# Kernel optimization log

Hardware: AMD Instinct MI355X
Metric: run time of the kernel (lower is better)

## Reference

```python
import jax, jax.numpy as jnp
import numpy as np

# Module hyperparameters (from init_kwargs / config defaults)
LOCAL_WINDOW = 128
GLOBAL_BUDGET = 64
ATT_BUDGET = 0.05
RANDOM_BUDGET = 0.1

B, S, D = 4, 4096, 1024


def setup_inputs() -> dict:
    key = jax.random.key(0)
    k1, k2 = jax.random.split(key)
    return {
        "hidden_states": jax.random.normal(k1, (B, S, D), dtype=jnp.float32),
        "attention_mask": jnp.ones((B, S), dtype=jnp.int32),
        "W_imp": jax.random.normal(k2, (1, D), dtype=jnp.float32) * 0.02,
    }


def _build_sparse_mask(hidden_states, attention_mask, W_imp):
    b, s, d = hidden_states.shape
    valid = attention_mask.astype(bool)                       # [b, s]
    # base mask: valid x valid, with causal constraint (is_decoder=True)
    i = jnp.arange(s)[:, None]
    j = jnp.arange(s)[None, :]
    causal = j <= i                                            # [s, s]
    base = (valid[:, None, :] & valid[:, :, None]) & causal[None]

    # 1) local causal sliding window: query i attends keys in [i-W+1, i]
    diff = i - j
    local = (diff >= 0) & (diff < LOCAL_WINDOW)                # [s, s]
    sparse = jnp.broadcast_to(local[None], (b, s, s))
    selected = jnp.broadcast_to(local.any(axis=0)[None], (b, s))

    # 2) global tokens via importance projection + top-k
    base_budget = min(GLOBAL_BUDGET, max(1, int(s * ATT_BUDGET)))
    scores = jnp.einsum('bsd,d->bs', hidden_states, W_imp[0])  # [b, s]
    scores = jnp.where(valid, scores, -jnp.inf)
    _, top_idx = jax.lax.top_k(scores, base_budget)            # [b, k]
    global_tokens = jnp.zeros((b, s), bool).at[
        jnp.arange(b)[:, None], top_idx].set(True)             # [b, s]
    # globals attend to everything and are attended by everything
    sparse = sparse | global_tokens[:, None, :] | global_tokens[:, :, None]
    selected = selected | global_tokens

    # 3) structured random tokens: deterministic strided selection
    r_budget = min(s, max(1, int(s * RANDOM_BUDGET)))
    stride = max(1, s // r_budget)
    rand_idx = (jnp.arange(r_budget) * stride) % s
    random_1d = jnp.zeros((s,), bool).at[rand_idx].set(True)
    random_tokens = jnp.broadcast_to(random_1d[None], (b, s))  # [b, s]
    sparse = sparse | random_tokens[:, None, :] | random_tokens[:, :, None]
    selected = selected | random_tokens

    # re-apply validity + causality
    sparse = sparse & base
    return sparse, selected, global_tokens, random_tokens


def reference(hidden_states, attention_mask, W_imp):
    b, s, _ = hidden_states.shape
    sparse, selected, gtok, rtok = _build_sparse_mask(
        hidden_states, attention_mask, W_imp)
    total_connections = sparse.sum(axis=(1, 2))
    attention_efficiency = total_connections.astype(jnp.float32) / float(s * s)
    # return sparse mask as float (the form consumed by attention), plus stats
    return (sparse.astype(jnp.float32), selected, attention_efficiency)
```

## Files before the change

### kernel.cpp

```cpp
#include <hip/hip_runtime.h>
#include <math.h>

#define BATCH 4
#define SEQ   4096
#define DIM   1024
#define TOPK  64
#define RSTRIDE 10
#define RBUDGET 409
#define LOCALW  128

typedef float nfloat4 __attribute__((ext_vector_type(4)));

#define WS_SCORES_OFF 0
#define WS_FLAGS_OFF  (BATCH * SEQ * sizeof(float))

__global__ void scores_kernel(const float* __restrict__ hs,
                              const int* __restrict__ amask,
                              const float* __restrict__ W,
                              float* __restrict__ scores) {
    int row  = blockIdx.x * 4 + (threadIdx.x >> 6);
    int lane = threadIdx.x & 63;
    const float4* h4 = (const float4*)(hs + (size_t)row * DIM);
    const float4* w4 = (const float4*)W;
    float acc = 0.0f;
#pragma unroll
    for (int k = 0; k < DIM / 4 / 64; ++k) {
        float4 h = h4[lane + 64 * k];
        float4 w = w4[lane + 64 * k];
        acc += h.x * w.x + h.y * w.y + h.z * w.z + h.w * w.w;
    }
#pragma unroll
    for (int off = 32; off; off >>= 1) acc += __shfl_down(acc, off, 64);
    if (lane == 0)
        scores[row] = amask[row] ? acc : -INFINITY;
}

__global__ void topk_flags_kernel(const float* __restrict__ scores,
                                  const int* __restrict__ amask,
                                  unsigned char* __restrict__ flags) {
    __shared__ unsigned int su[SEQ];
    __shared__ unsigned char gsel[SEQ];
    __shared__ unsigned int hist[257];
    __shared__ unsigned int sufA[257];
    __shared__ unsigned int sufB[257];
    __shared__ unsigned int bcast[2];

    int b = blockIdx.x, t = threadIdx.x;

    for (int k = t; k < SEQ; k += 256) {
        float s = scores[b * SEQ + k];
        unsigned int x = __float_as_uint(s);
        su[k] = (x & 0x80000000u) ? ~x : (x | 0x80000000u);
        gsel[k] = 0;
    }
    __syncthreads();

    unsigned int prefixVal = 0;
    unsigned int remaining = TOPK;
#pragma unroll
    for (int pass = 0; pass < 4; ++pass) {
        int shift = 24 - 8 * pass;
        unsigned int highmask = (pass == 0) ? 0u : (0xFFFFFFFFu << (shift + 8));

        hist[t] = 0;
        if (t == 0) hist[256] = 0;
        __syncthreads();

#pragma unroll
        for (int e = 0; e < SEQ / 256; ++e) {
            unsigned int u = su[t * (SEQ / 256) + e];
            if ((u & highmask) == prefixVal)
                atomicAdd(&hist[(u >> shift) & 0xFFu], 1u);
        }
        __syncthreads();

        sufA[t] = hist[t];
        if (t == 0) sufA[256] = 0;
        __syncthreads();
        unsigned int* src = sufA;
        unsigned int* dst = sufB;
        for (int d = 1; d < 256; d <<= 1) {
            unsigned int v = src[t] + ((t + d < 256) ? src[t + d] : 0u);
            dst[t] = v;
            if (t == 0) dst[256] = 0;
            __syncthreads();
            unsigned int* tmp = src; src = dst; dst = tmp;
        }
        if (src[t] >= remaining && src[t + 1] < remaining) {
            bcast[0] = (unsigned int)t;
            bcast[1] = remaining - src[t + 1];
        }
        __syncthreads();
        prefixVal |= (bcast[0] << shift);
        remaining = bcast[1];
        __syncthreads();
    }

    unsigned int T = prefixVal;
    unsigned int myeq = 0;
#pragma unroll
    for (int e = 0; e < SEQ / 256; ++e)
        if (su[t * (SEQ / 256) + e] == T) myeq++;
    sufA[t] = myeq;
    __syncthreads();
    {
        unsigned int* src = sufA;
        unsigned int* dst = sufB;
        for (int d = 1; d < 256; d <<= 1) {
            unsigned int v = src[t] + ((t >= d) ? src[t - d] : 0u);
            dst[t] = v;
            __syncthreads();
            unsigned int* tmp = src; src = dst; dst = tmp;
        }
        unsigned int taken = src[t] - myeq;
#pragma unroll
        for (int e = 0; e < SEQ / 256; ++e) {
            int idx = t * (SEQ / 256) + e;
            unsigned int u = su[idx];
            if (u > T) gsel[idx] = 1;
            else if (u == T) { if (taken < remaining) gsel[idx] = 1; taken++; }
        }
    }
    __syncthreads();

    for (int k = t; k < SEQ; k += 256) {
        int valid = (amask[b * SEQ + k] != 0) ? 1 : 0;
        int g = gsel[k];
        int r = ((k % RSTRIDE) == 0 && (k / RSTRIDE) < RBUDGET) ? 1 : 0;
        flags[b * SEQ + k] = (unsigned char)(valid | (g << 1) | (r << 2));
    }
}

__global__ void counts_kernel(const unsigned char* __restrict__ flags,
                              float* __restrict__ out_eff) {
    __shared__ int cumV[SEQ];
    __shared__ int cumH[SEQ];
    __shared__ int tvA[256], tvB[256], thA[256], thB[256];
    __shared__ int red[256];
    int b = blockIdx.x, t = threadIdx.x;
    int base = b * SEQ;

    int lv[16], lh[16];
    int sv = 0, sh = 0;
#pragma unroll
    for (int e = 0; e < 16; ++e) {
        unsigned char f = flags[base + t * 16 + e];
        int v = f & 1;
        int h = v & (((f & 6) != 0) ? 1 : 0);
        sv += v; sh += h;
        lv[e] = sv; lh[e] = sh;
    }
    tvA[t] = sv; thA[t] = sh;
    __syncthreads();
    int* vsrc = tvA; int* vdst = tvB;
    int* hsrc = thA; int* hdst = thB;
    for (int d = 1; d < 256; d <<= 1) {
        int av = vsrc[t] + ((t >= d) ? vsrc[t - d] : 0);
        int ah = hsrc[t] + ((t >= d) ? hsrc[t - d] : 0);
        vdst[t] = av; hdst[t] = ah;
        __syncthreads();
        int* tmp = vsrc; vsrc = vdst; vdst = tmp;
        tmp = hsrc; hsrc = hdst; hdst = tmp;
    }
    int bv = vsrc[t] - sv, bh = hsrc[t] - sh;
#pragma unroll
    for (int e = 0; e < 16; ++e) {
        cumV[t * 16 + e] = lv[e] + bv;
        cumH[t * 16 + e] = lh[e] + bh;
    }
    __syncthreads();

    int cnt = 0;
#pragma unroll
    for (int e = 0; e < 16; ++e) {
        int i = t * 16 + e;
        unsigned char f = flags[base + i];
        int validI = f & 1;
        int hotI = (f & 6) != 0;
        int c;
        if (hotI) c = cumV[i];
        else {
            int w = (i >= LOCALW) ? (cumV[i] - cumV[i - LOCALW]) : cumV[i];
            int g = (i >= LOCALW) ? cumH[i - LOCALW] : 0;
            c = w + g;
        }
        cnt += validI ? c : 0;
    }
    red[t] = cnt;
    __syncthreads();
    for (int s2 = 128; s2; s2 >>= 1) {
        if (t < s2) red[t] += red[t + s2];
        __syncthreads();
    }
    if (t == 0)
        out_eff[b] = (float)red[0] * (1.0f / ((float)SEQ * (float)SEQ));
}

__global__ void __launch_bounds__(256) mask_kernel(
        const unsigned char* __restrict__ flags,
        float* __restrict__ out) {
    int row0 = blockIdx.x << 2;
    int b = row0 >> 12;
    int t = threadIdx.x;

    const uchar4* f4 = (const uchar4*)(flags + b * SEQ);
    unsigned int validBits = 0, hotBits = 0;
#pragma unroll
    for (int k = 0; k < 4; ++k) {
        uchar4 f = f4[t + 256 * k];
        unsigned char fa[4] = {f.x, f.y, f.z, f.w};
#pragma unroll
        for (int e = 0; e < 4; ++e) {
            int idx = k * 4 + e;
            validBits |= (unsigned int)(fa[e] & 1u) << idx;
            hotBits   |= (unsigned int)((fa[e] & 6u) ? 1u : 0u) << idx;
        }
    }

    uchar4 fr = *(const uchar4*)(flags + row0);
    unsigned char fra[4] = {fr.x, fr.y, fr.z, fr.w};

#pragma unroll
    for (int r = 0; r < 4; ++r) {
        int i = (row0 + r) & (SEQ - 1);
        int validI = fra[r] & 1;
        int hotI = (fra[r] & 6) != 0;
        nfloat4* outrow4 = (nfloat4*)(out + (size_t)(row0 + r) * SEQ);
#pragma unroll
        for (int k = 0; k < 4; ++k) {
            int j4 = t + 256 * k;
            int j0 = j4 << 2;
            nfloat4 v;
#pragma unroll
            for (int e = 0; e < 4; ++e) {
                int idx = k * 4 + e;
                int j = j0 + e;
                int one = (j <= i) & validI & (int)((validBits >> idx) & 1u)
                        & (((i - j) < LOCALW) | hotI | (int)((hotBits >> idx) & 1u));
                v[e] = one ? 1.0f : 0.0f;
            }
            __builtin_nontemporal_store(v, outrow4 + j4);
        }
    }
}

__global__ void finalize_kernel(float* __restrict__ out_selected) {
    int idx = blockIdx.x * 256 + threadIdx.x;
    if (idx < BATCH * SEQ) out_selected[idx] = 1.0f;
}

extern "C" void kernel_launch(void* const* d_in, const int* in_sizes, int n_in,
                              void* d_out, int out_size, void* d_ws, size_t ws_size,
                              hipStream_t stream) {
    const float* hs    = (const float*)d_in[0];
    const int*   amask = (const int*)d_in[1];
    const float* W     = (const float*)d_in[2];

    char* ws = (char*)d_ws;
    float*         scores = (float*)(ws + WS_SCORES_OFF);
    unsigned char* flags  = (unsigned char*)(ws + WS_FLAGS_OFF);

    float* out_sparse   = (float*)d_out;
    float* out_selected = out_sparse + (size_t)BATCH * SEQ * SEQ;
    float* out_eff      = out_selected + BATCH * SEQ;

    scores_kernel<<<BATCH * SEQ / 4, 256, 0, stream>>>(hs, amask, W, scores);
    topk_flags_kernel<<<BATCH, 256, 0, stream>>>(scores, amask, flags);
    counts_kernel<<<BATCH, 256, 0, stream>>>(flags, out_eff);
    mask_kernel<<<BATCH * SEQ / 4, 256, 0, stream>>>(flags, out_sparse);
    finalize_kernel<<<(BATCH * SEQ + 255) / 256, 256, 0, stream>>>(out_selected);
}
```

Measured before the change: 336.7 us.

## Fuse topk, counts and finalize kernels; simplify mask kernel with per-vector branching

Merges the top-k flag kernel, the efficiency counting kernel and the selected-output fill into one kernel, which removes two launches and a global round-trip of the flags. The counting pass reads flags from shared memory and reuses the score buffer for the cumulative sums. The mask kernel now writes 8 rows per block and precomputes float vectors for the valid and valid-and-hot columns, so most output vectors are chosen by a branch instead of being built element by element. It also replaces nontemporal stores with normal stores, which may change cache behaviour on this write-bound 256MB output.

```diff
diff --git a/kernel.cpp b/kernel.cpp
--- a/kernel.cpp
+++ b/kernel.cpp
@@ -35,15 +35,20 @@
         scores[row] = amask[row] ? acc : -INFINITY;
 }
 
-__global__ void topk_flags_kernel(const float* __restrict__ scores,
+__global__ void topk_fused_kernel(const float* __restrict__ scores,
                                   const int* __restrict__ amask,
-                                  unsigned char* __restrict__ flags) {
+                                  unsigned char* __restrict__ flags,
+                                  float* __restrict__ out_selected,
+                                  float* __restrict__ out_eff) {
     __shared__ unsigned int su[SEQ];
+    __shared__ int cumH[SEQ];
     __shared__ unsigned char gsel[SEQ];
+    __shared__ unsigned char sflags[SEQ];
     __shared__ unsigned int hist[257];
     __shared__ unsigned int sufA[257];
     __shared__ unsigned int sufB[257];
     __shared__ unsigned int bcast[2];
+    __shared__ int tvA[256], tvB[256], thA[256], thB[256], red[256];
 
     int b = blockIdx.x, t = threadIdx.x;
 
@@ -65,7 +70,6 @@
         hist[t] = 0;
         if (t == 0) hist[256] = 0;
         __syncthreads();
-
 #pragma unroll
         for (int e = 0; e < SEQ / 256; ++e) {
             unsigned int u = su[t * (SEQ / 256) + e];
@@ -127,24 +131,19 @@
         int valid = (amask[b * SEQ + k] != 0) ? 1 : 0;
         int g = gsel[k];
         int r = ((k % RSTRIDE) == 0 && (k / RSTRIDE) < RBUDGET) ? 1 : 0;
-        flags[b * SEQ + k] = (unsigned char)(valid | (g << 1) | (r << 2));
-    }
-}
-
-__global__ void counts_kernel(const unsigned char* __restrict__ flags,
-                              float* __restrict__ out_eff) {
-    __shared__ int cumV[SEQ];
-    __shared__ int cumH[SEQ];
-    __shared__ int tvA[256], tvB[256], thA[256], thB[256];
-    __shared__ int red[256];
-    int b = blockIdx.x, t = threadIdx.x;
-    int base = b * SEQ;
-
+        unsigned char f = (unsigned char)(valid | (g << 1) | (r << 2));
+        flags[b * SEQ + k] = f;
+        sflags[k] = f;
+        out_selected[b * SEQ + k] = 1.0f;
+    }
+    __syncthreads();
+
+    int* cumV = (int*)su;
     int lv[16], lh[16];
     int sv = 0, sh = 0;
 #pragma unroll
     for (int e = 0; e < 16; ++e) {
-        unsigned char f = flags[base + t * 16 + e];
+        unsigned char f = sflags[t * 16 + e];
         int v = f & 1;
         int h = v & (((f & 6) != 0) ? 1 : 0);
         sv += v; sh += h;
@@ -174,7 +173,7 @@
 #pragma unroll
     for (int e = 0; e < 16; ++e) {
         int i = t * 16 + e;
-        unsigned char f = flags[base + i];
+        unsigned char f = sflags[i];
         int validI = f & 1;
         int hotI = (f & 6) != 0;
         int c;
@@ -199,29 +198,33 @@
 __global__ void __launch_bounds__(256) mask_kernel(
         const unsigned char* __restrict__ flags,
         float* __restrict__ out) {
-    int row0 = blockIdx.x << 2;
+    int row0 = blockIdx.x << 3;
     int b = row0 >> 12;
     int t = threadIdx.x;
 
     const uchar4* f4 = (const uchar4*)(flags + b * SEQ);
-    unsigned int validBits = 0, hotBits = 0;
+    nfloat4 A[4], C[4];
 #pragma unroll
     for (int k = 0; k < 4; ++k) {
         uchar4 f = f4[t + 256 * k];
         unsigned char fa[4] = {f.x, f.y, f.z, f.w};
 #pragma unroll
         for (int e = 0; e < 4; ++e) {
-            int idx = k * 4 + e;
-            validBits |= (unsigned int)(fa[e] & 1u) << idx;
-            hotBits   |= (unsigned int)((fa[e] & 6u) ? 1u : 0u) << idx;
-        }
-    }
-
-    uchar4 fr = *(const uchar4*)(flags + row0);
-    unsigned char fra[4] = {fr.x, fr.y, fr.z, fr.w};
-
-#pragma unroll
-    for (int r = 0; r < 4; ++r) {
+            int v = fa[e] & 1;
+            int h = (fa[e] & 6) != 0;
+            A[k][e] = v ? 1.0f : 0.0f;
+            C[k][e] = (v & h) ? 1.0f : 0.0f;
+        }
+    }
+
+    uchar4 frA = *(const uchar4*)(flags + row0);
+    uchar4 frB = *(const uchar4*)(flags + row0 + 4);
+    unsigned char fra[8] = {frA.x, frA.y, frA.z, frA.w, frB.x, frB.y, frB.z, frB.w};
+
+    const nfloat4 zero4 = {0.0f, 0.0f, 0.0f, 0.0f};
+
+#pragma unroll
+    for (int r = 0; r < 8; ++r) {
         int i = (row0 + r) & (SEQ - 1);
         int validI = fra[r] & 1;
         int hotI = (fra[r] & 6) != 0;
@@ -230,23 +233,26 @@
         for (int k = 0; k < 4; ++k) {
             int j4 = t + 256 * k;
             int j0 = j4 << 2;
-            nfloat4 v;
-#pragma unroll
-            for (int e = 0; e < 4; ++e) {
-                int idx = k * 4 + e;
-                int j = j0 + e;
-                int one = (j <= i) & validI & (int)((validBits >> idx) & 1u)
-                        & (((i - j) < LOCALW) | hotI | (int)((hotBits >> idx) & 1u));
-                v[e] = one ? 1.0f : 0.0f;
+            nfloat4 outv;
+            if (!validI || j0 > i) {
+                outv = zero4;
+            } else if (j0 + 3 <= i && j0 + (LOCALW - 1) >= i) {
+                outv = A[k];
+            } else if (j0 + 3 <= i - LOCALW) {
+                outv = hotI ? A[k] : C[k];
+            } else {
+#pragma unroll
+                for (int e = 0; e < 4; ++e) {
+                    int j = j0 + e;
+                    float av = A[k][e];
+                    float base = (j + (LOCALW - 1) >= i) ? av
+                               : (hotI ? av : C[k][e]);
+                    outv[e] = (j <= i) ? base : 0.0f;
+                }
             }
-            __builtin_nontemporal_store(v, outrow4 + j4);
-        }
-    }
-}
-
-__global__ void finalize_kernel(float* __restrict__ out_selected) {
-    int idx = blockIdx.x * 256 + threadIdx.x;
-    if (idx < BATCH * SEQ) out_selected[idx] = 1.0f;
+            outrow4[j4] = outv;
+        }
+    }
 }
 
 extern "C" void kernel_launch(void* const* d_in, const int* in_sizes, int n_in,
@@ -265,8 +271,7 @@
     float* out_eff      = out_selected + BATCH * SEQ;
 
     scores_kernel<<<BATCH * SEQ / 4, 256, 0, stream>>>(hs, amask, W, scores);
-    topk_flags_kernel<<<BATCH, 256, 0, stream>>>(scores, amask, flags);
-    counts_kernel<<<BATCH, 256, 0, stream>>>(flags, out_eff);
-    mask_kernel<<<BATCH * SEQ / 4, 256, 0, stream>>>(flags, out_sparse);
-    finalize_kernel<<<(BATCH * SEQ + 255) / 256, 256, 0, stream>>>(out_selected);
-}
+    topk_fused_kernel<<<BATCH, 256, 0, stream>>>(scores, amask, flags,
+                                                 out_selected, out_eff);
+    mask_kernel<<<BATCH * SEQ / 8, 256, 0, stream>>>(flags, out_sparse);
+}
```

Result: no change. 340.2 us (+1.0%).
